# Kernel tuning notes

Hardware: AMD Instinct MI355X
Metric: run time of the kernel (lower is better)

The kernel has to match this reference:

```python
import jax, jax.numpy as jnp
import numpy as np

N_NODES = 50000

def setup_inputs() -> dict:
    key = jax.random.key(0)
    k1, k2, k3, k4, k5 = jax.random.split(key, 5)
    x = jax.random.normal(k1, (4, N_NODES, 128), dtype=jnp.float32)
    weights = jax.random.normal(k2, (128, 64), dtype=jnp.float32) * (np.sqrt(2.0) * np.sqrt(6.0 / (128 + 64)))
    edge_vals = jax.random.uniform(k3, (800000,), dtype=jnp.float32)
    edge_rows = jax.random.randint(k4, (800000,), 0, N_NODES, dtype=jnp.int32)
    edge_cols = jax.random.randint(k5, (800000,), 0, N_NODES, dtype=jnp.int32)
    return {"x": x, "weights": weights, "edge_vals": edge_vals,
            "edge_rows": edge_rows, "edge_cols": edge_cols}

def reference(x, weights, edge_vals, edge_rows, edge_cols):
    # x: [B, N, Din]; weights: [Din, Dout]; adj as COO edges (shared across batch)
    pre = jnp.einsum('bni,io->bno', x, weights)          # dense GEMM per sample
    msg = pre[:, edge_cols, :] * edge_vals[None, :, None]  # [B, E, Dout] gather+scale
    # sparse adj @ pre: scatter-add messages to destination rows, per batch sample
    agg = jax.vmap(lambda m: jax.ops.segment_sum(m, edge_rows, num_segments=N_NODES))(msg)
    return jax.nn.relu(agg)
```

## Files before the change

kernel.cpp:

```cpp
#include <hip/hip_runtime.h>
#include <hip/hip_bf16.h>


#define B_BATCH 4
#define DIN 128
#define DOUT 64
#define CAP 64

typedef float f32x4 __attribute__((ext_vector_type(4)));
typedef short s16x8 __attribute__((ext_vector_type(8)));

static __device__ __forceinline__ unsigned short f2bf(float f) {
  unsigned u = __builtin_bit_cast(unsigned, f);
  unsigned r = (u + 0x7fff + ((u >> 16) & 1)) >> 16;
  return (unsigned short)r;
}
static __device__ __forceinline__ float lo16(unsigned u) {
  return __builtin_bit_cast(float, u << 16);
}
static __device__ __forceinline__ float hi16(unsigned u) {
  return __builtin_bit_cast(float, u & 0xffff0000u);
}

__global__ __launch_bounds__(256) void prep_wfrag_zero_kernel(
    const float* __restrict__ w, uint4* __restrict__ wimg,
    int* __restrict__ cnt, int n) {
  const int t = threadIdx.x;
  if (blockIdx.x != 0) {
    int i = (blockIdx.x - 1) * 256 + t;
    if (i < n) cnt[i] = 0;
    return;
  }
  for (int i = 0; i < 8; ++i) {
    int idx = i * 256 + t;
    int fslot = idx >> 6;
    int lane = idx & 63;
    int term = fslot & 1;
    int cks = fslot >> 1;
    int ct = cks >> 2, ks = cks & 3;
    int nn = ct * 16 + (lane & 15);
    int kb = ks * 32 + 4 * ((lane >> 4) & 3);
    unsigned short e[8];
#pragma unroll
    for (int j = 0; j < 8; ++j) {
      int k = kb + 16 * (j >> 2) + (j & 3);
      float wv = w[k * DOUT + nn];
      unsigned ub = __builtin_bit_cast(unsigned, wv);
      unsigned hib = ub & 0xffff0000u;
      if (term == 0) {
        e[j] = (unsigned short)(hib >> 16);
      } else {
        float lof = wv - __builtin_bit_cast(float, hib);
        e[j] = (unsigned short)(__builtin_bit_cast(unsigned, lof) >> 16);
      }
    }
    uint4 q;
    q.x = (unsigned)e[0] | ((unsigned)e[1] << 16);
    q.y = (unsigned)e[2] | ((unsigned)e[3] << 16);
    q.z = (unsigned)e[4] | ((unsigned)e[5] << 16);
    q.w = (unsigned)e[6] | ((unsigned)e[7] << 16);
    wimg[idx] = q;
  }
}

__global__ __launch_bounds__(256, 3) void gemm_fill_kernel(
    const float* __restrict__ x, const uint4* __restrict__ wimg,
    unsigned short* __restrict__ pre16, int NB16 , int nWaveTiles,
    const int* __restrict__ erows, const int* __restrict__ ecols,
    const float* __restrict__ evals, int* __restrict__ cnt,
    unsigned* __restrict__ epk, int nE) {
  const int t = threadIdx.x;
  const int wtile = blockIdx.x * 4 + (t >> 6);

  if (wtile < nWaveTiles) {
    const int lane = t & 63;
    const int rowg = (lane >> 4) & 3;
    const int rloc = lane & 15;

    const float* xp = x + (size_t)wtile * 32 * DIN + rloc * DIN + 4 * rowg;
    float4 X[2][4][2];
#pragma unroll
    for (int rs = 0; rs < 2; ++rs)
#pragma unroll
      for (int ks = 0; ks < 4; ++ks) {
        X[rs][ks][0] = *(const float4*)(xp + rs * 16 * DIN + ks * 32);
        X[rs][ks][1] = *(const float4*)(xp + rs * 16 * DIN + ks * 32 + 16);
      }

    f32x4 acc[2][4];
#pragma unroll
    for (int rs = 0; rs < 2; ++rs)
#pragma unroll
      for (int ct = 0; ct < 4; ++ct) acc[rs][ct] = (f32x4){0.f, 0.f, 0.f, 0.f};

#pragma unroll
    for (int ks = 0; ks < 4; ++ks) {
      s16x8 Bh[4], Bl[4];
#pragma unroll
      for (int ct = 0; ct < 4; ++ct) {
        const int fbase = (ct * 4 + ks) * 2;
        Bh[ct] = *(const s16x8*)&wimg[fbase * 64 + lane];
        Bl[ct] = *(const s16x8*)&wimg[(fbase + 1) * 64 + lane];
      }

      s16x8 Ah[2], Al[2];
#pragma unroll
      for (int rs = 0; rs < 2; ++rs) {
        float4 a0 = X[rs][ks][0];
        float4 a1 = X[rs][ks][1];

        unsigned b0 = __builtin_bit_cast(unsigned, a0.x);
        unsigned b1 = __builtin_bit_cast(unsigned, a0.y);
        unsigned b2 = __builtin_bit_cast(unsigned, a0.z);
        unsigned b3 = __builtin_bit_cast(unsigned, a0.w);
        unsigned c0 = __builtin_bit_cast(unsigned, a1.x);
        unsigned c1 = __builtin_bit_cast(unsigned, a1.y);
        unsigned c2 = __builtin_bit_cast(unsigned, a1.z);
        unsigned c3 = __builtin_bit_cast(unsigned, a1.w);

        union { s16x8 v; unsigned u[4]; } H, L;
        H.u[0] = (b0 >> 16) | (b1 & 0xffff0000u);
        H.u[1] = (b2 >> 16) | (b3 & 0xffff0000u);
        H.u[2] = (c0 >> 16) | (c1 & 0xffff0000u);
        H.u[3] = (c2 >> 16) | (c3 & 0xffff0000u);

        float l0 = a0.x - hi16(b0);
        float l1 = a0.y - hi16(b1);
        float l2 = a0.z - hi16(b2);
        float l3 = a0.w - hi16(b3);
        float l4 = a1.x - hi16(c0);
        float l5 = a1.y - hi16(c1);
        float l6 = a1.z - hi16(c2);
        float l7 = a1.w - hi16(c3);
        L.u[0] = (__builtin_bit_cast(unsigned, l0) >> 16) |
                 (__builtin_bit_cast(unsigned, l1) & 0xffff0000u);
        L.u[1] = (__builtin_bit_cast(unsigned, l2) >> 16) |
                 (__builtin_bit_cast(unsigned, l3) & 0xffff0000u);
        L.u[2] = (__builtin_bit_cast(unsigned, l4) >> 16) |
                 (__builtin_bit_cast(unsigned, l5) & 0xffff0000u);
        L.u[3] = (__builtin_bit_cast(unsigned, l6) >> 16) |
                 (__builtin_bit_cast(unsigned, l7) & 0xffff0000u);
        Ah[rs] = H.v;
        Al[rs] = L.v;
      }

#pragma unroll
      for (int ct = 0; ct < 4; ++ct) {
#pragma unroll
        for (int rs = 0; rs < 2; ++rs) {
          acc[rs][ct] = __builtin_amdgcn_mfma_f32_16x16x32_bf16(Ah[rs], Bh[ct], acc[rs][ct], 0, 0, 0);
          acc[rs][ct] = __builtin_amdgcn_mfma_f32_16x16x32_bf16(Ah[rs], Bl[ct], acc[rs][ct], 0, 0, 0);
          acc[rs][ct] = __builtin_amdgcn_mfma_f32_16x16x32_bf16(Al[rs], Bh[ct], acc[rs][ct], 0, 0, 0);
        }
      }
    }

#pragma unroll
    for (int rs = 0; rs < 2; ++rs) {
      int s = wtile * 2 + rs;
      int b = s / NB16;
      int nb = (s - b * NB16) * 16 + 4 * rowg;
#pragma unroll
      for (int r = 0; r < 4; ++r) {
        size_t o = (size_t)(nb + r) * 256 + b * 64 + rloc;
#pragma unroll
        for (int ct = 0; ct < 4; ++ct) {
          pre16[o + ct * 16] = f2bf(acc[rs][ct][r]);
        }
      }
    }
  }

  const int stride = gridDim.x * 256;
  for (int e = blockIdx.x * 256 + t; e < nE; e += stride) {
    int r = erows[e];
    int slot = atomicAdd(&cnt[r], 1);
    if (slot < CAP) {
      unsigned rec = ((unsigned)f2bf(evals[e]) << 16) | (unsigned)ecols[e];
      epk[r * CAP + slot] = rec;
    }
  }
}

__global__ __launch_bounds__(256) void gather_rows_kernel(
    const unsigned short* __restrict__ pre16, const int* __restrict__ cnt,
    const unsigned* __restrict__ epk, float* __restrict__ out, int N, int NS) {
  const int wid  = blockIdx.x * 4 + (threadIdx.x >> 6);
  const int lane = threadIdx.x & 63;
  if (wid >= N) return;

  const int m    = min(cnt[wid], CAP);
  const int eh   = lane >> 5;
  const int loff = ((lane >> 3) & 3) * 64 + (lane & 7) * 8;

  int   c = 0;
  float v = 0.0f;
  if (lane < m) {
    unsigned rec = epk[wid * CAP + lane];
    c = (int)(rec & 0xffffu);
    v = hi16(rec);
  }

  float a0 = 0.f, a1 = 0.f, a2 = 0.f, a3 = 0.f;
  float a4 = 0.f, a5 = 0.f, a6 = 0.f, a7 = 0.f;

  auto edge2 = [&](int j) {
    int   cj = __shfl(c, j + eh, 64);
    float vj = __shfl(v, j + eh, 64);
    const uint4 q = *(const uint4*)(pre16 + (size_t)cj * 256 + loff);
    a0 = fmaf(vj, lo16(q.x), a0);
    a1 = fmaf(vj, hi16(q.x), a1);
    a2 = fmaf(vj, lo16(q.y), a2);
    a3 = fmaf(vj, hi16(q.y), a3);
    a4 = fmaf(vj, lo16(q.z), a4);
    a5 = fmaf(vj, hi16(q.z), a5);
    a6 = fmaf(vj, lo16(q.w), a6);
    a7 = fmaf(vj, hi16(q.w), a7);
  };

  int j = 0;
  for (; j + 15 < m; j += 16) {
    edge2(j);      edge2(j + 2);  edge2(j + 4);  edge2(j + 6);
    edge2(j + 8);  edge2(j + 10); edge2(j + 12); edge2(j + 14);
  }
  for (; j + 7 < m; j += 8) { edge2(j); edge2(j + 2); edge2(j + 4); edge2(j + 6); }
  for (; j + 1 < m; j += 2) { edge2(j); }
  if (j < m) {
    int   cj = __shfl(c, j, 64);
    float vj = __shfl(v, j, 64);
    if (eh) vj = 0.0f;
    const uint4 q = *(const uint4*)(pre16 + (size_t)cj * 256 + loff);
    a0 = fmaf(vj, lo16(q.x), a0);
    a1 = fmaf(vj, hi16(q.x), a1);
    a2 = fmaf(vj, lo16(q.y), a2);
    a3 = fmaf(vj, hi16(q.y), a3);
    a4 = fmaf(vj, lo16(q.z), a4);
    a5 = fmaf(vj, hi16(q.z), a5);
    a6 = fmaf(vj, lo16(q.w), a6);
    a7 = fmaf(vj, hi16(q.w), a7);
  }

  a0 += __shfl_xor(a0, 32, 64);
  a1 += __shfl_xor(a1, 32, 64);
  a2 += __shfl_xor(a2, 32, 64);
  a3 += __shfl_xor(a3, 32, 64);
  a4 += __shfl_xor(a4, 32, 64);
  a5 += __shfl_xor(a5, 32, 64);
  a6 += __shfl_xor(a6, 32, 64);
  a7 += __shfl_xor(a7, 32, 64);

  if (lane < 32) {
    const int b   = lane >> 3;
    const int ch8 = (lane & 7) * 8;
    size_t o = (size_t)b * NS + (size_t)wid * DOUT + ch8;
    *(float4*)&out[o]     = make_float4(fmaxf(a0, 0.f), fmaxf(a1, 0.f),
                                        fmaxf(a2, 0.f), fmaxf(a3, 0.f));
    *(float4*)&out[o + 4] = make_float4(fmaxf(a4, 0.f), fmaxf(a5, 0.f),
                                        fmaxf(a6, 0.f), fmaxf(a7, 0.f));
  }
}

extern "C" void kernel_launch(void* const* d_in, const int* in_sizes, int n_in,
                              void* d_out, int out_size, void* d_ws, size_t ws_size,
                              hipStream_t stream) {
  const float* x     = (const float*)d_in[0];
  const float* w     = (const float*)d_in[1];
  const float* evals = (const float*)d_in[2];
  const int*   erows = (const int*)d_in[3];
  const int*   ecols = (const int*)d_in[4];
  float* out = (float*)d_out;

  const int N  = in_sizes[0] / (B_BATCH * DIN);
  const int E  = in_sizes[2];
  const int M  = B_BATCH * N;
  const int NS = N * DOUT;
  const int nWaveTiles = M / 32;
  const int NB16 = N / 16;

  size_t off = 0;
  auto alloc = [&](size_t bytes) {
    size_t o = off;
    off += (bytes + 255) & ~(size_t)255;
    return o;
  };
  size_t pre_off  = alloc((size_t)M * DOUT * 2);
  size_t wimg_off = alloc((size_t)2048 * 16);
  size_t cnt_off  = alloc((size_t)N * 4);
  size_t epk_off  = alloc((size_t)N * CAP * 4);
  (void)ws_size;

  char* ws = (char*)d_ws;
  unsigned short* pre16 = (unsigned short*)(ws + pre_off);
  uint4*    wimg = (uint4*)(ws + wimg_off);
  int*      cnt  = (int*)(ws + cnt_off);
  unsigned* epk  = (unsigned*)(ws + epk_off);

  prep_wfrag_zero_kernel<<<1 + (N + 255) / 256, 256, 0, stream>>>(w, wimg, cnt, N);

  gemm_fill_kernel<<<(nWaveTiles + 3) / 4, 256, 0, stream>>>(
      x, wimg, pre16, NB16, nWaveTiles, erows, ecols, evals, cnt, epk, E);

  gather_rows_kernel<<<(N + 3) / 4, 256, 0, stream>>>(pre16, cnt, epk, out, N, NS);
}
```

Baseline: 125.9 us.

## Fuse prep, GEMM/fill and gather into one cooperative persistent kernel

Result: slower. 362.5 us (+187.9%).

```diff
diff --git a/kernel.cpp b/kernel.cpp
--- a/kernel.cpp
+++ b/kernel.cpp
@@ -1,5 +1,8 @@
 #include <hip/hip_runtime.h>
 #include <hip/hip_bf16.h>
+#include <hip/hip_cooperative_groups.h>
+
+namespace cg = cooperative_groups;
 
 
 #define B_BATCH 4
@@ -22,17 +25,12 @@
   return __builtin_bit_cast(float, u & 0xffff0000u);
 }
 
-__global__ __launch_bounds__(256) void prep_wfrag_zero_kernel(
-    const float* __restrict__ w, uint4* __restrict__ wimg,
-    int* __restrict__ cnt, int n) {
-  const int t = threadIdx.x;
-  if (blockIdx.x != 0) {
-    int i = (blockIdx.x - 1) * 256 + t;
-    if (i < n) cnt[i] = 0;
-    return;
-  }
-  for (int i = 0; i < 8; ++i) {
-    int idx = i * 256 + t;
+static __device__ __forceinline__ void phase_prep(
+    int gtid, int nthr, const float* __restrict__ w, uint4* __restrict__ wimg,
+    int* __restrict__ cnt, int N) {
+  for (int i = gtid; i < N; i += nthr) cnt[i] = 0;
+  if (gtid < 2048) {
+    int idx = gtid;
     int fslot = idx >> 6;
     int lane = idx & 63;
     int term = fslot & 1;
@@ -63,20 +61,15 @@
   }
 }
 
-__global__ __launch_bounds__(256, 3) void gemm_fill_kernel(
-    const float* __restrict__ x, const uint4* __restrict__ wimg,
-    unsigned short* __restrict__ pre16, int NB16 , int nWaveTiles,
-    const int* __restrict__ erows, const int* __restrict__ ecols,
-    const float* __restrict__ evals, int* __restrict__ cnt,
-    unsigned* __restrict__ epk, int nE) {
-  const int t = threadIdx.x;
-  const int wtile = blockIdx.x * 4 + (t >> 6);
-
-  if (wtile < nWaveTiles) {
-    const int lane = t & 63;
-    const int rowg = (lane >> 4) & 3;
-    const int rloc = lane & 15;
-
+static __device__ __forceinline__ void phase_gemm(
+    int wstart, int wstride, const float* __restrict__ x,
+    const uint4* __restrict__ wimg, unsigned short* __restrict__ pre16,
+    int NB16, int nWaveTiles) {
+  const int lane = threadIdx.x & 63;
+  const int rowg = (lane >> 4) & 3;
+  const int rloc = lane & 15;
+
+  for (int wtile = wstart; wtile < nWaveTiles; wtile += wstride) {
     const float* xp = x + (size_t)wtile * 32 * DIN + rloc * DIN + 4 * rowg;
     float4 X[2][4][2];
 #pragma unroll
@@ -170,9 +163,13 @@
       }
     }
   }
-
-  const int stride = gridDim.x * 256;
-  for (int e = blockIdx.x * 256 + t; e < nE; e += stride) {
+}
+
+static __device__ __forceinline__ void phase_fill(
+    int gtid, int nthr, const int* __restrict__ erows,
+    const int* __restrict__ ecols, const float* __restrict__ evals,
+    int* __restrict__ cnt, unsigned* __restrict__ epk, int nE) {
+  for (int e = gtid; e < nE; e += nthr) {
     int r = erows[e];
     int slot = atomicAdd(&cnt[r], 1);
     if (slot < CAP) {
@@ -182,82 +179,130 @@
   }
 }
 
-__global__ __launch_bounds__(256) void gather_rows_kernel(
+static __device__ __forceinline__ void phase_gather(
+    int wstart, int wstride, const unsigned short* __restrict__ pre16,
+    const int* __restrict__ cnt, const unsigned* __restrict__ epk,
+    float* __restrict__ out, int N, int NS) {
+  const int lane = threadIdx.x & 63;
+  const int eh   = lane >> 5;
+  const int loff = ((lane >> 3) & 3) * 64 + (lane & 7) * 8;
+
+  for (int wid = wstart; wid < N; wid += wstride) {
+    const int m = min(cnt[wid], CAP);
+
+    int   c = 0;
+    float v = 0.0f;
+    if (lane < m) {
+      unsigned rec = epk[wid * CAP + lane];
+      c = (int)(rec & 0xffffu);
+      v = hi16(rec);
+    }
+
+    float a0 = 0.f, a1 = 0.f, a2 = 0.f, a3 = 0.f;
+    float a4 = 0.f, a5 = 0.f, a6 = 0.f, a7 = 0.f;
+
+    auto edge2 = [&](int j) {
+      int   cj = __shfl(c, j + eh, 64);
+      float vj = __shfl(v, j + eh, 64);
+      const uint4 q = *(const uint4*)(pre16 + (size_t)cj * 256 + loff);
+      a0 = fmaf(vj, lo16(q.x), a0);
+      a1 = fmaf(vj, hi16(q.x), a1);
+      a2 = fmaf(vj, lo16(q.y), a2);
+      a3 = fmaf(vj, hi16(q.y), a3);
+      a4 = fmaf(vj, lo16(q.z), a4);
+      a5 = fmaf(vj, hi16(q.z), a5);
+      a6 = fmaf(vj, lo16(q.w), a6);
+      a7 = fmaf(vj, hi16(q.w), a7);
+    };
+
+    int j = 0;
+    for (; j + 15 < m; j += 16) {
+      edge2(j);      edge2(j + 2);  edge2(j + 4);  edge2(j + 6);
+      edge2(j + 8);  edge2(j + 10); edge2(j + 12); edge2(j + 14);
+    }
+    for (; j + 7 < m; j += 8) { edge2(j); edge2(j + 2); edge2(j + 4); edge2(j + 6); }
+    for (; j + 1 < m; j += 2) { edge2(j); }
+    if (j < m) {
+      int   cj = __shfl(c, j, 64);
+      float vj = __shfl(v, j, 64);
+      if (eh) vj = 0.0f;
+      const uint4 q = *(const uint4*)(pre16 + (size_t)cj * 256 + loff);
+      a0 = fmaf(vj, lo16(q.x), a0);
+      a1 = fmaf(vj, hi16(q.x), a1);
+      a2 = fmaf(vj, lo16(q.y), a2);
+      a3 = fmaf(vj, hi16(q.y), a3);
+      a4 = fmaf(vj, lo16(q.z), a4);
+      a5 = fmaf(vj, hi16(q.z), a5);
+      a6 = fmaf(vj, lo16(q.w), a6);
+      a7 = fmaf(vj, hi16(q.w), a7);
+    }
+
+    a0 += __shfl_xor(a0, 32, 64);
+    a1 += __shfl_xor(a1, 32, 64);
+    a2 += __shfl_xor(a2, 32, 64);
+    a3 += __shfl_xor(a3, 32, 64);
+    a4 += __shfl_xor(a4, 32, 64);
+    a5 += __shfl_xor(a5, 32, 64);
+    a6 += __shfl_xor(a6, 32, 64);
+    a7 += __shfl_xor(a7, 32, 64);
+
+    if (lane < 32) {
+      const int b   = lane >> 3;
+      const int ch8 = (lane & 7) * 8;
+      size_t o = (size_t)b * NS + (size_t)wid * DOUT + ch8;
+      *(float4*)&out[o]     = make_float4(fmaxf(a0, 0.f), fmaxf(a1, 0.f),
+                                          fmaxf(a2, 0.f), fmaxf(a3, 0.f));
+      *(float4*)&out[o + 4] = make_float4(fmaxf(a4, 0.f), fmaxf(a5, 0.f),
+                                          fmaxf(a6, 0.f), fmaxf(a7, 0.f));
+    }
+  }
+}
+
+__global__ __launch_bounds__(256, 4) void fused_kernel(
+    const float* __restrict__ x, const float* __restrict__ w,
+    const int* __restrict__ erows, const int* __restrict__ ecols,
+    const float* __restrict__ evals, float* __restrict__ out,
+    unsigned short* __restrict__ pre16, uint4* __restrict__ wimg,
+    int* __restrict__ cnt, unsigned* __restrict__ epk,
+    int N, int E, int NS, int NB16, int nWaveTiles) {
+  cg::grid_group grid = cg::this_grid();
+  const int t = threadIdx.x;
+  const int gtid = blockIdx.x * 256 + t;
+  const int nthr = gridDim.x * 256;
+
+  phase_prep(gtid, nthr, w, wimg, cnt, N);
+  grid.sync();
+
+  phase_gemm(blockIdx.x * 4 + (t >> 6), gridDim.x * 4, x, wimg, pre16, NB16, nWaveTiles);
+  phase_fill(gtid, nthr, erows, ecols, evals, cnt, epk, E);
+  grid.sync();
+
+  phase_gather(blockIdx.x * 4 + (t >> 6), gridDim.x * 4, pre16, cnt, epk, out, N, NS);
+}
+
+__global__ __launch_bounds__(256) void prep_kernel(
+    const float* __restrict__ w, uint4* __restrict__ wimg,
+    int* __restrict__ cnt, int N) {
+  phase_prep(blockIdx.x * 256 + threadIdx.x, gridDim.x * 256, w, wimg, cnt, N);
+}
+
+__global__ __launch_bounds__(256, 3) void gemm_fill_kernel(
+    const float* __restrict__ x, const uint4* __restrict__ wimg,
+    unsigned short* __restrict__ pre16, int NB16, int nWaveTiles,
+    const int* __restrict__ erows, const int* __restrict__ ecols,
+    const float* __restrict__ evals, int* __restrict__ cnt,
+    unsigned* __restrict__ epk, int nE) {
+  phase_gemm(blockIdx.x * 4 + (threadIdx.x >> 6), gridDim.x * 4,
+             x, wimg, pre16, NB16, nWaveTiles);
+  phase_fill(blockIdx.x * 256 + threadIdx.x, gridDim.x * 256,
+             erows, ecols, evals, cnt, epk, nE);
+}
+
+__global__ __launch_bounds__(256) void gather_kernel(
     const unsigned short* __restrict__ pre16, const int* __restrict__ cnt,
     const unsigned* __restrict__ epk, float* __restrict__ out, int N, int NS) {
-  const int wid  = blockIdx.x * 4 + (threadIdx.x >> 6);
-  const int lane = threadIdx.x & 63;
-  if (wid >= N) return;
-
-  const int m    = min(cnt[wid], CAP);
-  const int eh   = lane >> 5;
-  const int loff = ((lane >> 3) & 3) * 64 + (lane & 7) * 8;
-
-  int   c = 0;
-  float v = 0.0f;
-  if (lane < m) {
-    unsigned rec = epk[wid * CAP + lane];
-    c = (int)(rec & 0xffffu);
-    v = hi16(rec);
-  }
-
-  float a0 = 0.f, a1 = 0.f, a2 = 0.f, a3 = 0.f;
-  float a4 = 0.f, a5 = 0.f, a6 = 0.f, a7 = 0.f;
-
-  auto edge2 = [&](int j) {
-    int   cj = __shfl(c, j + eh, 64);
-    float vj = __shfl(v, j + eh, 64);
-    const uint4 q = *(const uint4*)(pre16 + (size_t)cj * 256 + loff);
-    a0 = fmaf(vj, lo16(q.x), a0);
-    a1 = fmaf(vj, hi16(q.x), a1);
-    a2 = fmaf(vj, lo16(q.y), a2);
-    a3 = fmaf(vj, hi16(q.y), a3);
-    a4 = fmaf(vj, lo16(q.z), a4);
-    a5 = fmaf(vj, hi16(q.z), a5);
-    a6 = fmaf(vj, lo16(q.w), a6);
-    a7 = fmaf(vj, hi16(q.w), a7);
-  };
-
-  int j = 0;
-  for (; j + 15 < m; j += 16) {
-    edge2(j);      edge2(j + 2);  edge2(j + 4);  edge2(j + 6);
-    edge2(j + 8);  edge2(j + 10); edge2(j + 12); edge2(j + 14);
-  }
-  for (; j + 7 < m; j += 8) { edge2(j); edge2(j + 2); edge2(j + 4); edge2(j + 6); }
-  for (; j + 1 < m; j += 2) { edge2(j); }
-  if (j < m) {
-    int   cj = __shfl(c, j, 64);
-    float vj = __shfl(v, j, 64);
-    if (eh) vj = 0.0f;
-    const uint4 q = *(const uint4*)(pre16 + (size_t)cj * 256 + loff);
-    a0 = fmaf(vj, lo16(q.x), a0);
-    a1 = fmaf(vj, hi16(q.x), a1);
-    a2 = fmaf(vj, lo16(q.y), a2);
-    a3 = fmaf(vj, hi16(q.y), a3);
-    a4 = fmaf(vj, lo16(q.z), a4);
-    a5 = fmaf(vj, hi16(q.z), a5);
-    a6 = fmaf(vj, lo16(q.w), a6);
-    a7 = fmaf(vj, hi16(q.w), a7);
-  }
-
-  a0 += __shfl_xor(a0, 32, 64);
-  a1 += __shfl_xor(a1, 32, 64);
-  a2 += __shfl_xor(a2, 32, 64);
-  a3 += __shfl_xor(a3, 32, 64);
-  a4 += __shfl_xor(a4, 32, 64);
-  a5 += __shfl_xor(a5, 32, 64);
-  a6 += __shfl_xor(a6, 32, 64);
-  a7 += __shfl_xor(a7, 32, 64);
-
-  if (lane < 32) {
-    const int b   = lane >> 3;
-    const int ch8 = (lane & 7) * 8;
-    size_t o = (size_t)b * NS + (size_t)wid * DOUT + ch8;
-    *(float4*)&out[o]     = make_float4(fmaxf(a0, 0.f), fmaxf(a1, 0.f),
-                                        fmaxf(a2, 0.f), fmaxf(a3, 0.f));
-    *(float4*)&out[o + 4] = make_float4(fmaxf(a4, 0.f), fmaxf(a5, 0.f),
-                                        fmaxf(a6, 0.f), fmaxf(a7, 0.f));
-  }
+  phase_gather(blockIdx.x * 4 + (threadIdx.x >> 6), gridDim.x * 4,
+               pre16, cnt, epk, out, N, NS);
 }
 
 extern "C" void kernel_launch(void* const* d_in, const int* in_sizes, int n_in,
@@ -270,12 +315,12 @@
   const int*   ecols = (const int*)d_in[4];
   float* out = (float*)d_out;
 
-  const int N  = in_sizes[0] / (B_BATCH * DIN);
-  const int E  = in_sizes[2];
+  int N  = in_sizes[0] / (B_BATCH * DIN);
+  int E  = in_sizes[2];
   const int M  = B_BATCH * N;
-  const int NS = N * DOUT;
-  const int nWaveTiles = M / 32;
-  const int NB16 = N / 16;
+  int NS = N * DOUT;
+  int nWaveTiles = M / 32;
+  int NB16 = N / 16;
 
   size_t off = 0;
   auto alloc = [&](size_t bytes) {
@@ -295,10 +340,17 @@
   int*      cnt  = (int*)(ws + cnt_off);
   unsigned* epk  = (unsigned*)(ws + epk_off);
 
-  prep_wfrag_zero_kernel<<<1 + (N + 255) / 256, 256, 0, stream>>>(w, wimg, cnt, N);
-
-  gemm_fill_kernel<<<(nWaveTiles + 3) / 4, 256, 0, stream>>>(
-      x, wimg, pre16, NB16, nWaveTiles, erows, ecols, evals, cnt, epk, E);
-
-  gather_rows_kernel<<<(N + 3) / 4, 256, 0, stream>>>(pre16, cnt, epk, out, N, NS);
-}
+  void* args[] = {(void*)&x, (void*)&w, (void*)&erows, (void*)&ecols,
+                  (void*)&evals, (void*)&out, (void*)&pre16, (void*)&wimg,
+                  (void*)&cnt, (void*)&epk, (void*)&N, (void*)&E,
+                  (void*)&NS, (void*)&NB16, (void*)&nWaveTiles};
+  hipError_t err = hipLaunchCooperativeKernel(
+      (const void*)fused_kernel, dim3(1024), dim3(256), args, 0, stream);
+
+  if (err != hipSuccess) {
+    prep_kernel<<<1 + (N + 255) / 256, 256, 0, stream>>>(w, wimg, cnt, N);
+    gemm_fill_kernel<<<(nWaveTiles + 3) / 4, 256, 0, stream>>>(
+        x, wimg, pre16, NB16, nWaveTiles, erows, ecols, evals, cnt, epk, E);
+    gather_kernel<<<(N + 3) / 4, 256, 0, stream>>>(pre16, cnt, epk, out, N, NS);
+  }
+}
```
